# Kernel tuning notes

Measured on AMD Instinct MI355X. Metric: run time of the kernel, lower is better.

Reference implementation:

```python
import jax, jax.numpy as jnp
import numpy as np

DIM = 64   # voxel grid resolution per axis
C = 64     # channels (C_in == num_outputs, required by residual add)
N = 200000 # number of points
EPS = 1e-3 # keras BatchNormalization default epsilon

def _bn(x, g, b, m, v):
    # inference-mode batch norm
    return (x - m) * jax.lax.rsqrt(v + EPS) * g + b

def _conv3d_relu(x, k, b):
    # x: [1,X,Y,Z,Cin], k: [3,3,3,Cin,Cout] (DHWIO), 'same' padding, relu activation
    y = jax.lax.conv_general_dilated(x, k, (1, 1, 1), 'SAME',
        dimension_numbers=('NDHWC', 'DHWIO', 'NDHWC'))
    return jax.nn.relu(y + b)

def _trilinear(grid, pts):
    # grid: [X,Y,Z,C], pts: [N,3] in voxel coordinates
    dmax = jnp.asarray(grid.shape[:3], pts.dtype) - 1.0
    p = jnp.clip(pts, 0.0, dmax)
    f = jnp.floor(p)
    t = p - f  # [N,3] fractional part
    i0 = f.astype(jnp.int32)
    i1 = jnp.minimum(i0 + 1, jnp.asarray(grid.shape[:3], jnp.int32) - 1)
    out = jnp.zeros((pts.shape[0], grid.shape[-1]), grid.dtype)
    for dx in (0, 1):
        for dy in (0, 1):
            for dz in (0, 1):
                ix = i1[:, 0] if dx else i0[:, 0]
                iy = i1[:, 1] if dy else i0[:, 1]
                iz = i1[:, 2] if dz else i0[:, 2]
                w = ((t[:, 0] if dx else 1.0 - t[:, 0])
                     * (t[:, 1] if dy else 1.0 - t[:, 1])
                     * (t[:, 2] if dz else 1.0 - t[:, 2]))
                out = out + w[:, None] * grid[ix, iy, iz]
    return out

def setup_inputs():
    key = jax.random.key(0)
    ks = jax.random.split(key, 10)
    inputs = jax.random.normal(ks[0], (N, C), jnp.float32)
    # pt_coords already scaled into voxel space (VOXEL_SIZE_INV folded in)
    pt_coords = jax.random.uniform(ks[1], (N, 3), jnp.float32) * (DIM - 1)
    voxel_indexes = jax.random.randint(ks[2], (N, 3), 0, DIM)
    pts_per_voxel_inv = jax.random.uniform(ks[3], (1, DIM, DIM, DIM, 1), jnp.float32)
    s = 1.0 / np.sqrt(C)
    w_mlp = jax.random.normal(ks[4], (C, C), jnp.float32) * s
    b_mlp = jnp.zeros((C,), jnp.float32)
    sk = 1.0 / np.sqrt(27 * C)
    k1 = jax.random.normal(ks[5], (3, 3, 3, C, C), jnp.float32) * sk
    cb1 = jnp.zeros((C,), jnp.float32)
    k2 = jax.random.normal(ks[6], (3, 3, 3, C, C), jnp.float32) * sk
    cb2 = jnp.zeros((C,), jnp.float32)
    def bn_params(k):
        a, b_, c = jax.random.split(k, 3)
        g = 1.0 + 0.1 * jax.random.normal(a, (C,), jnp.float32)
        be = 0.1 * jax.random.normal(b_, (C,), jnp.float32)
        m = 0.1 * jax.random.normal(c, (C,), jnp.float32)
        v = jnp.ones((C,), jnp.float32)
        return g, be, m, v
    g0, be0, m0, v0 = bn_params(ks[7])
    g1, be1, m1, v1 = bn_params(ks[8])
    g2, be2, m2, v2 = bn_params(ks[9])
    return dict(inputs=inputs, pt_coords=pt_coords, voxel_indexes=voxel_indexes,
                pts_per_voxel_inv=pts_per_voxel_inv, w_mlp=w_mlp, b_mlp=b_mlp,
                g0=g0, be0=be0, m0=m0, v0=v0, k1=k1, cb1=cb1, g1=g1, be1=be1,
                m1=m1, v1=v1, k2=k2, cb2=cb2, g2=g2, be2=be2, m2=m2, v2=v2)

def reference(inputs, pt_coords, voxel_indexes, pts_per_voxel_inv, w_mlp, b_mlp,
              g0, be0, m0, v0, k1, cb1, g1, be1, m1, v1, k2, cb2, g2, be2, m2, v2):
    # point branch: Dense(relu) + BN
    mlp_out = _bn(jax.nn.relu(inputs @ w_mlp + b_mlp), g0, be0, m0, v0)
    # voxelize: scatter_nd adds duplicate-index contributions
    voxels = jnp.zeros((DIM, DIM, DIM, C), inputs.dtype).at[
        voxel_indexes[:, 0], voxel_indexes[:, 1], voxel_indexes[:, 2]].add(inputs)
    voxels = voxels[None] * pts_per_voxel_inv  # per-voxel mean normalization
    # voxel branch: two Conv3D(relu)+BN
    h = _bn(_conv3d_relu(voxels, k1, cb1), g1, be1, m1, v1)
    h = _bn(_conv3d_relu(h, k2, cb2), g2, be2, m2, v2)
    # devoxelize: trilinear gather back to points (coords already in voxel space)
    vox_out = _trilinear(h[0], pt_coords)
    return mlp_out + vox_out
```

## Files before the change

### kernel.cpp

```cpp
#include <hip/hip_runtime.h>
#include <hip/hip_bf16.h>

#define DIMV 64
#define CH 64
#define EPSB 1e-3f

using bf16x8 = __attribute__((ext_vector_type(8))) short;
using f32x16 = __attribute__((ext_vector_type(16))) float;

__device__ __forceinline__ unsigned short f2bf(float f) {
    union { float f; unsigned u; } x; x.f = f;
    unsigned r = x.u + 0x7fff + ((x.u >> 16) & 1);
    return (unsigned short)(r >> 16);
}
__device__ __forceinline__ float bf2f(unsigned short u) {
    union { unsigned u; float f; } x; x.u = ((unsigned)u) << 16;
    return x.f;
}

__global__ void scatter_kernel(const float* __restrict__ x, const int* __restrict__ idx,
                               float* __restrict__ grid, int n_total) {
    int tid = blockIdx.x * blockDim.x + threadIdx.x;
    if (tid >= n_total) return;
    int n = tid >> 6, c = tid & 63;
    int ix = idx[n * 3 + 0], iy = idx[n * 3 + 1], iz = idx[n * 3 + 2];
    atomicAdd(&grid[(size_t)(((ix * DIMV) + iy) * DIMV + iz) * CH + c], x[tid]);
}

__global__ void pack_kernel(const float* __restrict__ A, const float* __restrict__ inv,
                            unsigned short* __restrict__ G1) {
    int t = blockIdx.x * 256 + threadIdx.x;
    if (t >= (DIMV * DIMV * DIMV * CH) / 8) return;
    int v = t >> 3, c8 = (t & 7) * 8;
    const float* src = A + (size_t)v * CH + c8;
    float s = inv[v];
    __align__(16) unsigned short tmp[8];
#pragma unroll
    for (int j = 0; j < 8; ++j) tmp[j] = f2bf(src[j] * s);
    *(int4*)(G1 + (size_t)t * 8) = *(const int4*)tmp;
}

__global__ void wprep_all(const float* __restrict__ K1, const float* __restrict__ K2,
                          const float* __restrict__ Wm, unsigned short* __restrict__ wbuf1,
                          unsigned short* __restrict__ wbuf2, unsigned short* __restrict__ wm) {
    int t = blockIdx.x * 256 + threadIdx.x;
    if (t >= 2 * 110592 + 4096) return;
    const float* src;
    unsigned short* dst;
    int tt;
    if (t < 110592) { src = K1; dst = wbuf1; tt = t; }
    else if (t < 221184) { src = K2; dst = wbuf2; tt = t - 110592; }
    else { src = Wm; dst = wm; tt = t - 221184; }
    int j = tt & 7;
    int l = (tt >> 3) & 63;
    int nt = (tt >> 9) & 1;
    int kkl = (tt >> 10) & 3;
    int d = tt >> 12;
    int ci = kkl * 16 + (l >> 5) * 8 + j;
    int co = nt * 32 + (l & 31);
    dst[tt] = f2bf(src[((size_t)d * 64 + ci) * 64 + co]);
}

__global__ __launch_bounds__(512) void conv_mfma(
    const unsigned short* __restrict__ G, const unsigned short* __restrict__ wbuf,
    const float* __restrict__ cb, const float* __restrict__ g,
    const float* __restrict__ be, const float* __restrict__ m,
    const float* __restrict__ v, unsigned short* __restrict__ out) {
    __shared__ __align__(16) unsigned short slab[612 * 128];
    const int tid = threadIdx.x;
    const int lane = tid & 63;
    const int w = tid >> 6;
    const int cx = w >> 1;
    const int cy0 = 2 * (w & 1);
    const int lz = lane & 31;
    const int kg = lane >> 5;
    const int BX = blockIdx.x, BY = blockIdx.y, BZ = blockIdx.z;
    const int x0 = 4 * BX - 1, y0 = 4 * BY - 1;
    const int zbase = 32 * BZ - 1;

    for (int it = 0; it < 20; ++it) {
        int idx = it * 512 + tid;
        if (idx < 9792) {
            int s = idx & 15;
            int r = idx >> 4;
            int zp = r % 17;
            int ryx = r / 17;
            int xx = x0 + ryx / 6;
            int yy = y0 + ryx % 6;
            int cp = s ^ (zp & 15);
            int c = cp >> 1, p = cp & 1;
            int zz = zbase + 2 * zp + p;
            int4 val = make_int4(0, 0, 0, 0);
            if ((unsigned)xx < DIMV && (unsigned)yy < DIMV && (unsigned)zz < DIMV)
                val = *(const int4*)(G + (size_t)(((xx * DIMV) + yy) * DIMV + zz) * CH + c * 8);
            *(int4*)(slab + (size_t)idx * 8) = val;
        }
    }
    __syncthreads();

    f32x16 acc[2][2];
#pragma unroll
    for (int ct = 0; ct < 2; ++ct)
#pragma unroll
        for (int nt = 0; nt < 2; ++nt)
#pragma unroll
            for (int r = 0; r < 16; ++r) acc[ct][nt][r] = 0.f;

    bf16x8 bfr0[8], bfr1[8];
#pragma unroll
    for (int q = 0; q < 8; ++q)
        bfr0[q] = *(const bf16x8*)(wbuf + q * 512 + lane * 8);

#pragma unroll
    for (int d = 0; d < 27; ++d) {
        if (d < 26) {
            const unsigned short* wn = wbuf + (size_t)(d + 1) * 4096;
            if (d & 1) {
#pragma unroll
                for (int q = 0; q < 8; ++q) bfr0[q] = *(const bf16x8*)(wn + q * 512 + lane * 8);
            } else {
#pragma unroll
                for (int q = 0; q < 8; ++q) bfr1[q] = *(const bf16x8*)(wn + q * 512 + lane * 8);
            }
        }
        const int dx = d / 9, dy = (d / 3) % 3, dz = d % 3;
        const int zval = lz + dz;
        const int zp = zval >> 1, p = zval & 1;
        const int rbase = ((cx + dx) * 6 + (cy0 + dy)) * 17 + zp;
#pragma unroll
        for (int kkl = 0; kkl < 4; ++kkl) {
            const int c = kkl * 2 + kg;
            const int slot = (c * 2 + p) ^ (zp & 15);
            bf16x8 a0 = *(const bf16x8*)(slab + rbase * 128 + slot * 8);
            bf16x8 a1 = *(const bf16x8*)(slab + (rbase + 17) * 128 + slot * 8);
            bf16x8 b0 = (d & 1) ? bfr1[kkl * 2 + 0] : bfr0[kkl * 2 + 0];
            bf16x8 b1 = (d & 1) ? bfr1[kkl * 2 + 1] : bfr0[kkl * 2 + 1];
            acc[0][0] = __builtin_amdgcn_mfma_f32_32x32x16_bf16(a0, b0, acc[0][0], 0, 0, 0);
            acc[1][0] = __builtin_amdgcn_mfma_f32_32x32x16_bf16(a1, b0, acc[1][0], 0, 0, 0);
            acc[0][1] = __builtin_amdgcn_mfma_f32_32x32x16_bf16(a0, b1, acc[0][1], 0, 0, 0);
            acc[1][1] = __builtin_amdgcn_mfma_f32_32x32x16_bf16(a1, b1, acc[1][1], 0, 0, 0);
        }
    }

    const int x_out = 4 * BX + cx;
#pragma unroll
    for (int ct = 0; ct < 2; ++ct) {
        int y_out = 4 * BY + cy0 + ct;
#pragma unroll
        for (int nt = 0; nt < 2; ++nt) {
            int co = nt * 32 + lz;
            float scale = g[co] * rsqrtf(v[co] + EPSB);
            float shift = be[co] - m[co] * scale;
            float bias = cb[co];
            size_t base = (size_t)((x_out * DIMV) + y_out) * DIMV * CH + co;
#pragma unroll
            for (int r = 0; r < 16; ++r) {
                int zrow = (r & 3) + 8 * (r >> 2) + 4 * kg;
                int z = BZ * 32 + zrow;
                float val = fmaxf(acc[ct][nt][r] + bias, 0.f) * scale + shift;
                out[base + (size_t)z * CH] = f2bf(val);
            }
        }
    }
}

__global__ __launch_bounds__(256) void mlp_gather(
    const float* __restrict__ x, const unsigned short* __restrict__ wfrag,
    const float* __restrict__ b, const float* __restrict__ g,
    const float* __restrict__ be, const float* __restrict__ m,
    const float* __restrict__ v, const unsigned short* __restrict__ grid,
    const float* __restrict__ pts, float* __restrict__ out, int npts) {
    __shared__ float lds[128 * 64];
    const int w = threadIdx.x >> 6;
    const int lane = threadIdx.x & 63;
    const int col = lane & 31;
    const int kg = lane >> 5;
    const int p0 = (blockIdx.x * 4 + w) * 32;

    if (p0 < npts) {
        bf16x8 a[4];
        const float* xr = x + (size_t)(p0 + col) * CH + kg * 8;
#pragma unroll
        for (int kk = 0; kk < 4; ++kk) {
            const float* p = xr + kk * 16;
            bf16x8 t;
#pragma unroll
            for (int j = 0; j < 8; ++j) t[j] = (short)f2bf(p[j]);
            a[kk] = t;
        }
        f32x16 acc[2];
#pragma unroll
        for (int nt = 0; nt < 2; ++nt)
#pragma unroll
            for (int r = 0; r < 16; ++r) acc[nt][r] = 0.f;
#pragma unroll
        for (int kk = 0; kk < 4; ++kk) {
            bf16x8 b0 = *(const bf16x8*)(wfrag + (kk * 2 + 0) * 512 + lane * 8);
            bf16x8 b1 = *(const bf16x8*)(wfrag + (kk * 2 + 1) * 512 + lane * 8);
            acc[0] = __builtin_amdgcn_mfma_f32_32x32x16_bf16(a[kk], b0, acc[0], 0, 0, 0);
            acc[1] = __builtin_amdgcn_mfma_f32_32x32x16_bf16(a[kk], b1, acc[1], 0, 0, 0);
        }
#pragma unroll
        for (int nt = 0; nt < 2; ++nt) {
            int co = nt * 32 + col;
            float scale = g[co] * rsqrtf(v[co] + EPSB);
            float shift = be[co] - m[co] * scale;
            float bias = b[co];
#pragma unroll
            for (int r = 0; r < 16; ++r) {
                int row = (r & 3) + 8 * (r >> 2) + 4 * kg;
                float val = fmaxf(acc[nt][r] + bias, 0.f) * scale + shift;
                lds[(w * 32 + row) * 64 + co] = val;
            }
        }
    }
    __syncthreads();

    const int pblk = blockIdx.x * 128;
#pragma unroll 4
    for (int i = 0; i < 32; ++i) {
        int idx = i * 256 + threadIdx.x;
        int pl = idx >> 6;
        int c = idx & 63;
        int pt = pblk + pl;
        if (pt >= npts) break;
        float px = fminf(fmaxf(pts[pt * 3 + 0], 0.f), (float)(DIMV - 1));
        float py = fminf(fmaxf(pts[pt * 3 + 1], 0.f), (float)(DIMV - 1));
        float pz = fminf(fmaxf(pts[pt * 3 + 2], 0.f), (float)(DIMV - 1));
        float fx = floorf(px), fy = floorf(py), fz = floorf(pz);
        float tx = px - fx, ty = py - fy, tz = pz - fz;
        int x0 = (int)fx, y0 = (int)fy, z0 = (int)fz;
        int x1 = min(x0 + 1, DIMV - 1), y1 = min(y0 + 1, DIMV - 1), z1 = min(z0 + 1, DIMV - 1);
        float wx0 = 1.f - tx, wy0 = 1.f - ty, wz0 = 1.f - tz;
        float acc = lds[pl * 64 + c];
        acc = fmaf(wx0 * wy0 * wz0, bf2f(grid[(size_t)(((x0 * DIMV) + y0) * DIMV + z0) * CH + c]), acc);
        acc = fmaf(wx0 * wy0 * tz,  bf2f(grid[(size_t)(((x0 * DIMV) + y0) * DIMV + z1) * CH + c]), acc);
        acc = fmaf(wx0 * ty * wz0,  bf2f(grid[(size_t)(((x0 * DIMV) + y1) * DIMV + z0) * CH + c]), acc);
        acc = fmaf(wx0 * ty * tz,   bf2f(grid[(size_t)(((x0 * DIMV) + y1) * DIMV + z1) * CH + c]), acc);
        acc = fmaf(tx * wy0 * wz0,  bf2f(grid[(size_t)(((x1 * DIMV) + y0) * DIMV + z0) * CH + c]), acc);
        acc = fmaf(tx * wy0 * tz,   bf2f(grid[(size_t)(((x1 * DIMV) + y0) * DIMV + z1) * CH + c]), acc);
        acc = fmaf(tx * ty * wz0,   bf2f(grid[(size_t)(((x1 * DIMV) + y1) * DIMV + z0) * CH + c]), acc);
        acc = fmaf(tx * ty * tz,    bf2f(grid[(size_t)(((x1 * DIMV) + y1) * DIMV + z1) * CH + c]), acc);
        out[(size_t)pt * CH + c] = acc;
    }
}

extern "C" void kernel_launch(void* const* d_in, const int* in_sizes, int n_in,
                              void* d_out, int out_size, void* d_ws, size_t ws_size,
                              hipStream_t stream) {
    const float* inputs = (const float*)d_in[0];
    const float* pt_coords = (const float*)d_in[1];
    const int* voxel_indexes = (const int*)d_in[2];
    const float* ppvi = (const float*)d_in[3];
    const float* w_mlp = (const float*)d_in[4];
    const float* b_mlp = (const float*)d_in[5];
    const float* g0 = (const float*)d_in[6];
    const float* be0 = (const float*)d_in[7];
    const float* m0 = (const float*)d_in[8];
    const float* v0 = (const float*)d_in[9];
    const float* k1 = (const float*)d_in[10];
    const float* cb1 = (const float*)d_in[11];
    const float* g1 = (const float*)d_in[12];
    const float* be1 = (const float*)d_in[13];
    const float* m1 = (const float*)d_in[14];
    const float* v1 = (const float*)d_in[15];
    const float* k2 = (const float*)d_in[16];
    const float* cb2 = (const float*)d_in[17];
    const float* g2 = (const float*)d_in[18];
    const float* be2 = (const float*)d_in[19];
    const float* m2 = (const float*)d_in[20];
    const float* v2 = (const float*)d_in[21];
    float* out = (float*)d_out;

    char* ws = (char*)d_ws;
    float* A = (float*)ws;
    unsigned short* G2 = (unsigned short*)ws;
    unsigned short* G3 = (unsigned short*)(ws + 33554432);
    unsigned short* G1 = (unsigned short*)(ws + 67108864);
    unsigned short* wbuf1 = (unsigned short*)(ws + 100663296);
    unsigned short* wbuf2 = (unsigned short*)(ws + 100884480);
    unsigned short* wmlp = (unsigned short*)(ws + 101105664);

    const int n_total = in_sizes[0];
    const int npts = n_total / CH;
    const int nblk = (n_total + 255) / 256;
    const size_t grid_elems = (size_t)DIMV * DIMV * DIMV * CH;

    hipMemsetAsync(A, 0, grid_elems * sizeof(float), stream);
    wprep_all<<<880, 256, 0, stream>>>(k1, k2, w_mlp, wbuf1, wbuf2, wmlp);
    scatter_kernel<<<nblk, 256, 0, stream>>>(inputs, voxel_indexes, A, n_total);
    pack_kernel<<<(int)(grid_elems / 8 + 255) / 256, 256, 0, stream>>>(A, ppvi, G1);

    dim3 cgrid(16, 16, 2);
    conv_mfma<<<cgrid, 512, 0, stream>>>(G1, wbuf1, cb1, g1, be1, m1, v1, G2);
    conv_mfma<<<cgrid, 512, 0, stream>>>(G2, wbuf2, cb2, g2, be2, m2, v2, G3);

    mlp_gather<<<(npts + 127) / 128, 256, 0, stream>>>(
        inputs, wmlp, b_mlp, g0, be0, m0, v0, G3, pt_coords, out, npts);
}
```

Before: 279.3 us.

## Shrink conv3d block tile to 2x2 columns with one accumulator per wave

Reworks the MFMA conv kernel so each block covers a 2x2 x-y footprint instead of 4x4, with each wave computing one output column and one 32-channel half. The smaller LDS slab and fewer accumulator registers are meant to raise occupancy and the number of blocks in flight. In exchange, halo reloading grows, and each A and weight fragment is reused by only one MFMA instead of two, increasing LDS and global/L2 traffic per FLOP.

New measurement: 296.0 us. 6.0% more time.

```diff
diff --git a/kernel.cpp b/kernel.cpp
--- a/kernel.cpp
+++ b/kernel.cpp
@@ -66,27 +66,29 @@
     const float* __restrict__ cb, const float* __restrict__ g,
     const float* __restrict__ be, const float* __restrict__ m,
     const float* __restrict__ v, unsigned short* __restrict__ out) {
-    __shared__ __align__(16) unsigned short slab[612 * 128];
+    __shared__ __align__(16) unsigned short slab[272 * 128];
     const int tid = threadIdx.x;
     const int lane = tid & 63;
     const int w = tid >> 6;
-    const int cx = w >> 1;
-    const int cy0 = 2 * (w & 1);
+    const int cx = (w >> 2) & 1;
+    const int cy = (w >> 1) & 1;
+    const int ntw = w & 1;
     const int lz = lane & 31;
     const int kg = lane >> 5;
     const int BX = blockIdx.x, BY = blockIdx.y, BZ = blockIdx.z;
-    const int x0 = 4 * BX - 1, y0 = 4 * BY - 1;
+    const int x0 = 2 * BX - 1, y0 = 2 * BY - 1;
     const int zbase = 32 * BZ - 1;
 
-    for (int it = 0; it < 20; ++it) {
+#pragma unroll
+    for (int it = 0; it < 9; ++it) {
         int idx = it * 512 + tid;
-        if (idx < 9792) {
+        if (idx < 4352) {
             int s = idx & 15;
             int r = idx >> 4;
             int zp = r % 17;
-            int ryx = r / 17;
-            int xx = x0 + ryx / 6;
-            int yy = y0 + ryx % 6;
+            int rxy = r / 17;
+            int xx = x0 + (rxy >> 2);
+            int yy = y0 + (rxy & 3);
             int cp = s ^ (zp & 15);
             int c = cp >> 1, p = cp & 1;
             int zz = zbase + 2 * zp + p;
@@ -98,69 +100,54 @@
     }
     __syncthreads();
 
-    f32x16 acc[2][2];
-#pragma unroll
-    for (int ct = 0; ct < 2; ++ct)
-#pragma unroll
-        for (int nt = 0; nt < 2; ++nt)
-#pragma unroll
-            for (int r = 0; r < 16; ++r) acc[ct][nt][r] = 0.f;
-
-    bf16x8 bfr0[8], bfr1[8];
-#pragma unroll
-    for (int q = 0; q < 8; ++q)
-        bfr0[q] = *(const bf16x8*)(wbuf + q * 512 + lane * 8);
+    f32x16 acc;
+#pragma unroll
+    for (int r = 0; r < 16; ++r) acc[r] = 0.f;
+
+    bf16x8 bfr0[4], bfr1[4];
+#pragma unroll
+    for (int q = 0; q < 4; ++q)
+        bfr0[q] = *(const bf16x8*)(wbuf + q * 1024 + ntw * 512 + lane * 8);
 
 #pragma unroll
     for (int d = 0; d < 27; ++d) {
         if (d < 26) {
-            const unsigned short* wn = wbuf + (size_t)(d + 1) * 4096;
+            const unsigned short* wn = wbuf + (size_t)(d + 1) * 4096 + ntw * 512 + lane * 8;
             if (d & 1) {
 #pragma unroll
-                for (int q = 0; q < 8; ++q) bfr0[q] = *(const bf16x8*)(wn + q * 512 + lane * 8);
+                for (int q = 0; q < 4; ++q) bfr0[q] = *(const bf16x8*)(wn + q * 1024);
             } else {
 #pragma unroll
-                for (int q = 0; q < 8; ++q) bfr1[q] = *(const bf16x8*)(wn + q * 512 + lane * 8);
+                for (int q = 0; q < 4; ++q) bfr1[q] = *(const bf16x8*)(wn + q * 1024);
             }
         }
         const int dx = d / 9, dy = (d / 3) % 3, dz = d % 3;
         const int zval = lz + dz;
         const int zp = zval >> 1, p = zval & 1;
-        const int rbase = ((cx + dx) * 6 + (cy0 + dy)) * 17 + zp;
+        const int rbase = ((cx + dx) * 4 + (cy + dy)) * 17 + zp;
 #pragma unroll
         for (int kkl = 0; kkl < 4; ++kkl) {
             const int c = kkl * 2 + kg;
             const int slot = (c * 2 + p) ^ (zp & 15);
-            bf16x8 a0 = *(const bf16x8*)(slab + rbase * 128 + slot * 8);
-            bf16x8 a1 = *(const bf16x8*)(slab + (rbase + 17) * 128 + slot * 8);
-            bf16x8 b0 = (d & 1) ? bfr1[kkl * 2 + 0] : bfr0[kkl * 2 + 0];
-            bf16x8 b1 = (d & 1) ? bfr1[kkl * 2 + 1] : bfr0[kkl * 2 + 1];
-            acc[0][0] = __builtin_amdgcn_mfma_f32_32x32x16_bf16(a0, b0, acc[0][0], 0, 0, 0);
-            acc[1][0] = __builtin_amdgcn_mfma_f32_32x32x16_bf16(a1, b0, acc[1][0], 0, 0, 0);
-            acc[0][1] = __builtin_amdgcn_mfma_f32_32x32x16_bf16(a0, b1, acc[0][1], 0, 0, 0);
-            acc[1][1] = __builtin_amdgcn_mfma_f32_32x32x16_bf16(a1, b1, acc[1][1], 0, 0, 0);
-        }
-    }
-
-    const int x_out = 4 * BX + cx;
-#pragma unroll
-    for (int ct = 0; ct < 2; ++ct) {
-        int y_out = 4 * BY + cy0 + ct;
-#pragma unroll
-        for (int nt = 0; nt < 2; ++nt) {
-            int co = nt * 32 + lz;
-            float scale = g[co] * rsqrtf(v[co] + EPSB);
-            float shift = be[co] - m[co] * scale;
-            float bias = cb[co];
-            size_t base = (size_t)((x_out * DIMV) + y_out) * DIMV * CH + co;
-#pragma unroll
-            for (int r = 0; r < 16; ++r) {
-                int zrow = (r & 3) + 8 * (r >> 2) + 4 * kg;
-                int z = BZ * 32 + zrow;
-                float val = fmaxf(acc[ct][nt][r] + bias, 0.f) * scale + shift;
-                out[base + (size_t)z * CH] = f2bf(val);
-            }
-        }
+            bf16x8 a = *(const bf16x8*)(slab + rbase * 128 + slot * 8);
+            bf16x8 b = (d & 1) ? bfr1[kkl] : bfr0[kkl];
+            acc = __builtin_amdgcn_mfma_f32_32x32x16_bf16(a, b, acc, 0, 0, 0);
+        }
+    }
+
+    const int x_out = 2 * BX + cx;
+    const int y_out = 2 * BY + cy;
+    const int co = ntw * 32 + lz;
+    float scale = g[co] * rsqrtf(v[co] + EPSB);
+    float shift = be[co] - m[co] * scale;
+    float bias = cb[co];
+    size_t base = (size_t)((x_out * DIMV) + y_out) * DIMV * CH + co;
+#pragma unroll
+    for (int r = 0; r < 16; ++r) {
+        int zrow = (r & 3) + 8 * (r >> 2) + 4 * kg;
+        int z = BZ * 32 + zrow;
+        float val = fmaxf(acc[r] + bias, 0.f) * scale + shift;
+        out[base + (size_t)z * CH] = f2bf(val);
     }
 }
 
@@ -291,7 +278,7 @@
     scatter_kernel<<<nblk, 256, 0, stream>>>(inputs, voxel_indexes, A, n_total);
     pack_kernel<<<(int)(grid_elems / 8 + 255) / 256, 256, 0, stream>>>(A, ppvi, G1);
 
-    dim3 cgrid(16, 16, 2);
+    dim3 cgrid(32, 32, 2);
     conv_mfma<<<cgrid, 512, 0, stream>>>(G1, wbuf1, cb1, g1, be1, m1, v1, G2);
     conv_mfma<<<cgrid, 512, 0, stream>>>(G2, wbuf2, cb2, g2, be2, m2, v2, G3);
 
```
